# Kernel optimization log

Measured on AMD Instinct MI355X. Metric: run time of the kernel, lower is better.

Reference implementation:

```python
import jax, jax.numpy as jnp
import numpy as np

MODES = 4
WIDTH = 8
IN_CH = 3
OUT_CH = 6
LAMBDA_RES = 0.3


def spectral_conv3d(x, w1, w2, w3, w4):
    # x: [B, C, D, H, W] real. Standard FNO3d SpectralConv3d:
    # rfftn over last 3 dims, multiply low modes in 4 corner octants, irfftn.
    B, C, D, H, W = x.shape
    m = MODES
    x_ft = jnp.fft.rfftn(x, axes=(-3, -2, -1))  # [B,C,D,H,W//2+1] complex

    def mul(blk, w):
        return jnp.einsum('bixyz,ioxyz->boxyz', blk, w)

    out_ft = jnp.zeros((B, w1.shape[1], D, H, W // 2 + 1), dtype=x_ft.dtype)
    out_ft = out_ft.at[:, :, :m, :m, :m].set(mul(x_ft[:, :, :m, :m, :m], w1))
    out_ft = out_ft.at[:, :, -m:, :m, :m].set(mul(x_ft[:, :, -m:, :m, :m], w2))
    out_ft = out_ft.at[:, :, :m, -m:, :m].set(mul(x_ft[:, :, :m, -m:, :m], w3))
    out_ft = out_ft.at[:, :, -m:, -m:, :m].set(mul(x_ft[:, :, -m:, -m:, :m], w4))
    return jnp.fft.irfftn(out_ft, s=(D, H, W), axes=(-3, -2, -1))


def fno3d(u, fc0_w, fc0_b, spec_ws, conv_ws, conv_bs, fc1_w, fc1_b, fc2_w, fc2_b):
    # Lift: 1x1 conv via einsum (channels-first)
    x = jnp.einsum('bcdhw,oc->bodhw', u, fc0_w) + fc0_b[None, :, None, None, None]
    for i in range(4):
        w1, w2, w3, w4 = spec_ws[i]
        x1 = spectral_conv3d(x, w1, w2, w3, w4)
        x2 = jnp.einsum('bcdhw,oc->bodhw', x, conv_ws[i]) + conv_bs[i][None, :, None, None, None]
        x = x1 + x2
        if i < 3:
            x = jax.nn.gelu(x)
    x = jnp.einsum('bcdhw,oc->bodhw', x, fc1_w) + fc1_b[None, :, None, None, None]
    x = jax.nn.gelu(x)
    x = jnp.einsum('bcdhw,oc->bodhw', x, fc2_w) + fc2_b[None, :, None, None, None]
    return x


def setup_inputs() -> dict:
    key = jax.random.key(0)
    ks = jax.random.split(key, 32)
    B, D, H, W = 8, 64, 64, 64
    m, wd = MODES, WIDTH
    u = jax.random.normal(ks[0], (B, IN_CH, D, H, W), dtype=jnp.float32)
    scale = 1.0 / (wd * wd)
    spec_ws = []
    ki = 1
    for _ in range(4):
        layer = []
        for _ in range(4):
            re = jax.random.uniform(ks[ki], (wd, wd, m, m, m)) * scale
            im = jax.random.uniform(ks[ki + 1], (wd, wd, m, m, m)) * scale
            layer.append(re + 1j * im)
            ki += 2
        spec_ws.append(tuple(layer))
    conv_ws = [jax.random.normal(ks[ki + i], (wd, wd)) * (1.0 / wd) for i in range(4)]
    ki += 4
    conv_bs = [jnp.zeros((wd,), jnp.float32) for _ in range(4)]
    fc0_w = jax.random.normal(ks[ki], (wd, IN_CH)) * 0.3; ki += 1
    fc0_b = jnp.zeros((wd,), jnp.float32)
    fc1_w = jax.random.normal(ks[ki], (4 * wd, wd)) * 0.2; ki += 1
    fc1_b = jnp.zeros((4 * wd,), jnp.float32)
    fc2_w = jax.random.normal(ks[ki], (OUT_CH, 4 * wd)) * 0.2; ki += 1
    fc2_b = jnp.zeros((OUT_CH,), jnp.float32)
    nu = jnp.asarray(0.001, jnp.float32)
    return {
        'u': u, 'nu': nu,
        'fc0_w': fc0_w, 'fc0_b': fc0_b,
        'spec_ws': spec_ws, 'conv_ws': conv_ws, 'conv_bs': conv_bs,
        'fc1_w': fc1_w, 'fc1_b': fc1_b, 'fc2_w': fc2_w, 'fc2_b': fc2_b,
    }


def reference(u, nu, fc0_w, fc0_b, spec_ws, conv_ws, conv_bs, fc1_w, fc1_b, fc2_w, fc2_b):
    B, C, D, H, W = u.shape
    # hard core: zeros [B,6,D,H,W] with first 3 channels = u*nu
    hard = jnp.concatenate([u * nu, jnp.zeros((B, 3, D, H, W), u.dtype)], axis=1)
    soft = fno3d(u, fc0_w, fc0_b, spec_ws, conv_ws, conv_bs, fc1_w, fc1_b, fc2_w, fc2_b)
    return hard + LAMBDA_RES * soft
```

## Files before the change

kernel.cpp:

```cpp
#include <hip/hip_runtime.h>


#define TWO_PI_OVER_64 0.09817477042468103

__device__ __forceinline__ float gelu_fast(float x) {
    float x2 = x * x;
    float p  = x * (1.0f + 0.044715f * x2);
    float e  = __builtin_amdgcn_exp2f(-2.3022083f * p);
    return x * __builtin_amdgcn_rcpf(1.0f + e);
}

#define BUILD_TW() \
    __shared__ float twc[64], tws[64]; \
    if (threadIdx.x < 64) { \
        double a_ = TWO_PI_OVER_64 * (double)threadIdx.x; \
        twc[threadIdx.x] = (float)cos(a_); tws[threadIdx.x] = (float)sin(a_); \
    }

__device__ __forceinline__ void a_tail_lds(
    const float v[4], const float c1[4], const float s1[4],
    const float c2[4], const float s2[4], const float c3[4], const float s3[4],
    int wq, float4* __restrict__ AslRow)
{
    float p0  = v[0] + v[1] + v[2] + v[3];
    float ar1 = v[0]*c1[0] + v[1]*c1[1] + v[2]*c1[2] + v[3]*c1[3];
    float ai1 = -(v[0]*s1[0] + v[1]*s1[1] + v[2]*s1[2] + v[3]*s1[3]);
    float ar2 = v[0]*c2[0] + v[1]*c2[1] + v[2]*c2[2] + v[3]*c2[3];
    float ai2 = -(v[0]*s2[0] + v[1]*s2[1] + v[2]*s2[2] + v[3]*s2[3]);
    float ar3 = v[0]*c3[0] + v[1]*c3[1] + v[2]*c3[2] + v[3]*c3[3];
    float ai3 = -(v[0]*s3[0] + v[1]*s3[1] + v[2]*s3[2] + v[3]*s3[3]);
    #pragma unroll
    for (int m = 1; m < 16; m <<= 1) {
        p0  += __shfl_xor(p0,  m);
        ar1 += __shfl_xor(ar1, m);  ai1 += __shfl_xor(ai1, m);
        ar2 += __shfl_xor(ar2, m);  ai2 += __shfl_xor(ai2, m);
        ar3 += __shfl_xor(ar3, m);  ai3 += __shfl_xor(ai3, m);
    }
    if (wq < 2) {
        float4 av;
        av.x = (wq == 0) ? p0   : ar2;
        av.y = (wq == 0) ? 0.f  : ai2;
        av.z = (wq == 0) ? ar1  : ar3;
        av.w = (wq == 0) ? ai1  : ai3;
        AslRow[wq] = av;
    }
}

__device__ __forceinline__ void h_partial_atomic(
    const float2* __restrict__ Asl, const float* __restrict__ twc,
    const float* __restrict__ tws, int t, int b, int dx, int dy0,
    float2* __restrict__ Bh)
{
    const int kz = t & 3, ky = (t >> 2) & 7, o = t >> 5;
    const int kyv = ky < 4 ? ky : ky + 56;
    float re = 0.f, im = 0.f;
    int ti = (kyv * dy0) & 63;
    #pragma unroll
    for (int dyl = 0; dyl < 16; ++dyl) {
        float2 a = Asl[(o * 16 + dyl) * 4 + kz];
        float cc = twc[ti], ss = tws[ti];
        re += a.x * cc + a.y * ss;
        im += a.y * cc - a.x * ss;
        ti = (ti + kyv) & 63;
    }
    float* p = (float*)&Bh[(size_t)(b * 8 + o) * 2048 + dx * 32 + ky * 4 + kz];
    atomicAdd(p, re);
    atomicAdd(p + 1, im);
}

__global__ __launch_bounds__(256) void k_liftA(
    const float* __restrict__ u, const float* __restrict__ fc0w,
    const float* __restrict__ fc0b, float* __restrict__ x,
    float2* __restrict__ Bh)
{
    BUILD_TW();
    __shared__ float4 Asl4[8 * 16 * 2];
    const int t = threadIdx.x, bid = blockIdx.x;
    const int b = bid >> 8, dx = (bid >> 2) & 63, dy0 = (bid & 3) * 16;
    const int dyl = t >> 4, wq = t & 15;
    const size_t sp = (size_t)dx * 4096 + (size_t)(dy0 + dyl) * 64 + wq * 4;
    float uin[3][4];
    #pragma unroll
    for (int c = 0; c < 3; ++c) {
        float4 v = *(const float4*)&u[(size_t)(b * 3 + c) * 262144 + sp];
        uin[c][0] = v.x; uin[c][1] = v.y; uin[c][2] = v.z; uin[c][3] = v.w;
    }
    __syncthreads();
    float c1[4], s1[4], c2[4], s2[4], c3[4], s3[4];
    #pragma unroll
    for (int j = 0; j < 4; ++j) {
        int w = wq * 4 + j;
        c1[j] = twc[w];             s1[j] = tws[w];
        c2[j] = twc[(2 * w) & 63];  s2[j] = tws[(2 * w) & 63];
        c3[j] = twc[(3 * w) & 63];  s3[j] = tws[(3 * w) & 63];
    }
    #pragma unroll
    for (int o = 0; o < 8; ++o) {
        float w0 = fc0w[o * 3 + 0], w1 = fc0w[o * 3 + 1], w2 = fc0w[o * 3 + 2];
        float bb = fc0b[o];
        float v[4];
        #pragma unroll
        for (int j = 0; j < 4; ++j)
            v[j] = bb + uin[0][j] * w0 + uin[1][j] * w1 + uin[2][j] * w2;
        *(float4*)&x[(size_t)(b * 8 + o) * 262144 + sp] =
            make_float4(v[0], v[1], v[2], v[3]);
        a_tail_lds(v, c1, s1, c2, s2, c3, s3, wq, &Asl4[(o * 16 + dyl) * 2]);
    }
    __syncthreads();
    h_partial_atomic((const float2*)Asl4, twc, tws, t, b, dx, dy0, Bh);
}

__global__ __launch_bounds__(256) void k_fDmix(
    const float2* __restrict__ Bh,
    const float2* __restrict__ w1, const float2* __restrict__ w2,
    const float2* __restrict__ w3, const float2* __restrict__ w4,
    float2* __restrict__ O)
{
    BUILD_TW();
    __shared__ float2 Cs[256];
    const int t = threadIdx.x, bid = blockIdx.x;
    const int b = bid >> 3, kx = bid & 7;
    const int kxv = kx < 4 ? kx : kx + 56;
    __syncthreads();
    {
        int kz = t & 3, ky = (t >> 2) & 7, c = t >> 5;
        const float2* Bp = Bh + (size_t)(b * 8 + c) * 2048 + ky * 4 + kz;
        float re = 0.f, im = 0.f;
        int ti = 0;
        #pragma unroll 8
        for (int dx = 0; dx < 64; ++dx) {
            float2 v = Bp[dx * 32];
            float cc = twc[ti], ss = tws[ti];
            re += v.x * cc + v.y * ss;
            im += v.y * cc - v.x * ss;
            ti = (ti + kxv) & 63;
        }
        Cs[t] = make_float2(re, im);
    }
    __syncthreads();
    {
        int kz = t & 3, ky = (t >> 2) & 7, o = t >> 5;
        const float2* wsel = (kx < 4) ? ((ky < 4) ? w1 : w3) : ((ky < 4) ? w2 : w4);
        int kxw = kx & 3, kyw = ky & 3;
        float re = 0.f, im = 0.f;
        #pragma unroll
        for (int i = 0; i < 8; ++i) {
            float2 cv = Cs[i * 32 + ky * 4 + kz];
            float2 wv = wsel[(((size_t)(i * 8 + o) * 4 + kxw) * 4 + kyw) * 4 + kz];
            re += cv.x * wv.x - cv.y * wv.y;
            im += cv.x * wv.y + cv.y * wv.x;
        }
        O[(((size_t)(b * 8 + o) * 8 + kx) * 8 + ky) * 4 + kz] = make_float2(re, im);
    }
}

__global__ __launch_bounds__(256) void k_ptA(
    float* __restrict__ x, const float2* __restrict__ O,
    const float* __restrict__ cw, const float* __restrict__ cb,
    float2* __restrict__ Bh)
{
    BUILD_TW();
    __shared__ float2 Ps[256];
    __shared__ float2 Qs[8 * 16 * 4];
    __shared__ float4 Asl4[8 * 16 * 2];
    const int t = threadIdx.x, bid = blockIdx.x;
    const int b = bid >> 8, dx = (bid >> 2) & 63, dy0 = (bid & 3) * 16;
    const int dyl = t >> 4, wq = t & 15;
    const size_t sp = (size_t)dx * 4096 + (size_t)(dy0 + dyl) * 64 + wq * 4;
    float4 xv[8];
    #pragma unroll
    for (int c = 0; c < 8; ++c)
        xv[c] = *(const float4*)&x[(size_t)(b * 8 + c) * 262144 + sp];
    const int pkz = t & 3, pky = (t >> 2) & 7, po = t >> 5;
    float2 ov[8];
    #pragma unroll
    for (int kxi = 0; kxi < 8; ++kxi)
        ov[kxi] = O[(((size_t)(b * 8 + po) * 8 + kxi) * 8 + pky) * 4 + pkz];
    __syncthreads();
    {
        float re = 0.f, im = 0.f;
        #pragma unroll
        for (int kxi = 0; kxi < 8; ++kxi) {
            int kxv = kxi < 4 ? kxi : kxi + 56;
            int ti = (kxv * dx) & 63;
            float cc = twc[ti], ss = tws[ti];
            re += ov[kxi].x * cc - ov[kxi].y * ss;
            im += ov[kxi].y * cc + ov[kxi].x * ss;
        }
        Ps[t] = make_float2(re, im);
    }
    __syncthreads();
    for (int it = t; it < 512; it += 256) {
        int kz = it & 3, qdyl = (it >> 2) & 15, o = it >> 6;
        int dy = dy0 + qdyl;
        float re = 0.f, im = 0.f;
        #pragma unroll
        for (int kyi = 0; kyi < 8; ++kyi) {
            int kyv = kyi < 4 ? kyi : kyi + 56;
            int ti = (kyv * dy) & 63;
            float2 v = Ps[(o * 8 + kyi) * 4 + kz];
            float cc = twc[ti], ss = tws[ti];
            re += v.x * cc - v.y * ss;
            im += v.y * cc + v.x * ss;
        }
        Qs[(o * 16 + qdyl) * 4 + kz] = make_float2(re, im);
    }
    __syncthreads();
    float c1[4], s1[4], c2[4], s2[4], c3[4], s3[4];
    #pragma unroll
    for (int j = 0; j < 4; ++j) {
        int w = wq * 4 + j;
        c1[j] = twc[w];             s1[j] = tws[w];
        c2[j] = twc[(2 * w) & 63];  s2[j] = tws[(2 * w) & 63];
        c3[j] = twc[(3 * w) & 63];  s3[j] = tws[(3 * w) & 63];
    }
    const float invN3 = 1.0f / 262144.0f;
    #pragma unroll
    for (int o = 0; o < 8; ++o) {
        float4 qa = *(const float4*)&Qs[(o * 16 + dyl) * 4];
        float4 qb = *(const float4*)&Qs[(o * 16 + dyl) * 4 + 2];
        float outj[4];
        #pragma unroll
        for (int j = 0; j < 4; ++j) {
            float x1 = qa.x + 2.f * (qa.z * c1[j] - qa.w * s1[j]
                                   + qb.x * c2[j] - qb.y * s2[j]
                                   + qb.z * c3[j] - qb.w * s3[j]);
            x1 *= invN3;
            float x2 = cb[o];
            #pragma unroll
            for (int c = 0; c < 8; ++c) {
                const float* xc = &xv[c].x;
                x2 += cw[o * 8 + c] * xc[j];
            }
            outj[j] = gelu_fast(x1 + x2);
        }
        *(float4*)&x[(size_t)(b * 8 + o) * 262144 + sp] =
            make_float4(outj[0], outj[1], outj[2], outj[3]);
        a_tail_lds(outj, c1, s1, c2, s2, c3, s3, wq, &Asl4[(o * 16 + dyl) * 2]);
    }
    __syncthreads();
    h_partial_atomic((const float2*)Asl4, twc, tws, t, b, dx, dy0, Bh);
}

__global__ __launch_bounds__(256) void k_ptout(
    const float* __restrict__ x, const float2* __restrict__ O,
    const float* __restrict__ cw, const float* __restrict__ cb,
    const float* __restrict__ u, const float* __restrict__ nu,
    const float* __restrict__ fc1w, const float* __restrict__ fc1b,
    const float* __restrict__ fc2w, const float* __restrict__ fc2b,
    float* __restrict__ out)
{
    BUILD_TW();
    __shared__ float2 Ps[256];
    __shared__ float2 Qs[8 * 8 * 4];
    const int t = threadIdx.x, bid = blockIdx.x;
    const int b = bid >> 9, dx = (bid >> 3) & 63, dy0 = (bid & 7) * 8;
    const int dyl = t >> 5, wp = t & 31;
    const size_t sp = (size_t)dx * 4096 + (size_t)(dy0 + dyl) * 64 + wp * 2;
    float2 xv[8];
    #pragma unroll
    for (int c = 0; c < 8; ++c)
        xv[c] = *(const float2*)&x[(size_t)(b * 8 + c) * 262144 + sp];
    float2 uv[3];
    #pragma unroll
    for (int c = 0; c < 3; ++c)
        uv[c] = *(const float2*)&u[(size_t)(b * 3 + c) * 262144 + sp];
    const int pkz = t & 3, pky = (t >> 2) & 7, po = t >> 5;
    float2 ovv[8];
    #pragma unroll
    for (int kxi = 0; kxi < 8; ++kxi)
        ovv[kxi] = O[(((size_t)(b * 8 + po) * 8 + kxi) * 8 + pky) * 4 + pkz];
    __syncthreads();
    {
        float re = 0.f, im = 0.f;
        #pragma unroll
        for (int kxi = 0; kxi < 8; ++kxi) {
            int kxv = kxi < 4 ? kxi : kxi + 56;
            int ti = (kxv * dx) & 63;
            float cc = twc[ti], ss = tws[ti];
            re += ovv[kxi].x * cc - ovv[kxi].y * ss;
            im += ovv[kxi].y * cc + ovv[kxi].x * ss;
        }
        Ps[t] = make_float2(re, im);
    }
    __syncthreads();
    {
        int kz = t & 3, qdyl = (t >> 2) & 7, o = t >> 5;
        int dy = dy0 + qdyl;
        float re = 0.f, im = 0.f;
        #pragma unroll
        for (int kyi = 0; kyi < 8; ++kyi) {
            int kyv = kyi < 4 ? kyi : kyi + 56;
            int ti = (kyv * dy) & 63;
            float2 v = Ps[(o * 8 + kyi) * 4 + kz];
            float cc = twc[ti], ss = tws[ti];
            re += v.x * cc - v.y * ss;
            im += v.y * cc + v.x * ss;
        }
        Qs[(o * 8 + qdyl) * 4 + kz] = make_float2(re, im);
    }
    __syncthreads();
    float c1[2], s1[2], c2[2], s2[2], c3[2], s3[2];
    #pragma unroll
    for (int j = 0; j < 2; ++j) {
        int w = wp * 2 + j;
        c1[j] = twc[w];             s1[j] = tws[w];
        c2[j] = twc[(2 * w) & 63];  s2[j] = tws[(2 * w) & 63];
        c3[j] = twc[(3 * w) & 63];  s3[j] = tws[(3 * w) & 63];
    }
    const float invN3 = 1.0f / 262144.0f;
    float vv[8][2];
    #pragma unroll
    for (int o = 0; o < 8; ++o) {
        float4 qa = *(const float4*)&Qs[(o * 8 + dyl) * 4];
        float4 qb = *(const float4*)&Qs[(o * 8 + dyl) * 4 + 2];
        #pragma unroll
        for (int j = 0; j < 2; ++j) {
            float x1 = qa.x + 2.f * (qa.z * c1[j] - qa.w * s1[j]
                                   + qb.x * c2[j] - qb.y * s2[j]
                                   + qb.z * c3[j] - qb.w * s3[j]);
            x1 *= invN3;
            float x2 = cb[o];
            #pragma unroll
            for (int c = 0; c < 8; ++c) {
                const float* xc = &xv[c].x;
                x2 += cw[o * 8 + c] * xc[j];
            }
            vv[o][j] = x1 + x2;
        }
    }
    float so[6][2];
    #pragma unroll
    for (int c6 = 0; c6 < 6; ++c6)
        #pragma unroll
        for (int j = 0; j < 2; ++j) so[c6][j] = fc2b[c6];
    #pragma unroll 4
    for (int h = 0; h < 32; ++h) {
        float wr[8];
        #pragma unroll
        for (int c = 0; c < 8; ++c) wr[c] = fc1w[h * 8 + c];
        const float hb = fc1b[h];
        float w2r[6];
        #pragma unroll
        for (int c6 = 0; c6 < 6; ++c6) w2r[c6] = fc2w[c6 * 32 + h];
        #pragma unroll
        for (int j = 0; j < 2; ++j) {
            float a = hb;
            #pragma unroll
            for (int c = 0; c < 8; ++c) a += vv[c][j] * wr[c];
            float g = gelu_fast(a);
            #pragma unroll
            for (int c6 = 0; c6 < 6; ++c6) so[c6][j] += g * w2r[c6];
        }
    }
    const float nuv = nu[0];
    #pragma unroll
    for (int c6 = 0; c6 < 6; ++c6) {
        float2 res;
        if (c6 < 3) {
            res.x = 0.3f * so[c6][0] + uv[c6].x * nuv;
            res.y = 0.3f * so[c6][1] + uv[c6].y * nuv;
        } else {
            res.x = 0.3f * so[c6][0];
            res.y = 0.3f * so[c6][1];
        }
        *(float2*)&out[(size_t)(b * 6 + c6) * 262144 + sp] = res;
    }
}

__global__ void k_pack(const float* __restrict__ re, const float* __restrict__ im,
                       float2* __restrict__ dst)
{
    int i = blockIdx.x * 256 + threadIdx.x;
    if (i < 4096) dst[i] = make_float2(re[i], im[i]);
}

extern "C" void kernel_launch(void* const* d_in, const int* in_sizes, int n_in,
                              void* d_out, int out_size, void* d_ws, size_t ws_size,
                              hipStream_t stream)
{
    (void)out_size;
    const char* leaf[32];
    bool spec_split = false;
    const char* spec_re[16]; const char* spec_im[16];
    int src = 0;
    leaf[0] = (const char*)d_in[src++];
    leaf[1] = (const char*)d_in[src++];
    leaf[2] = (const char*)d_in[src++];
    leaf[3] = (const char*)d_in[src++];
    {
        int s = (src < n_in) ? in_sizes[src] : 4096;
        if (n_in >= 48 && s == 4096) {
            spec_split = true;
            for (int i = 0; i < 16; ++i) {
                spec_re[i] = (const char*)d_in[src++];
                spec_im[i] = (const char*)d_in[src++];
            }
        } else {
            int per;
            if (s == 4096 || s == 8192) per = 1;
            else if (s == 16384 || s == 32768) per = 4;
            else per = 16;
            for (int i = 0; i < 16; i += per) {
                const char* base = (const char*)d_in[src++];
                for (int j = 0; j < per; ++j) leaf[4 + i + j] = base + (size_t)j * 4096 * 8;
            }
        }
    }
    {
        int s = (src < n_in) ? in_sizes[src] : 64;
        if (s == 64) { for (int i = 0; i < 4; ++i) leaf[20 + i] = (const char*)d_in[src++]; }
        else { const char* base = (const char*)d_in[src++];
               for (int i = 0; i < 4; ++i) leaf[20 + i] = base + (size_t)i * 64 * 4; }
    }
    {
        int s = (src < n_in) ? in_sizes[src] : 8;
        if (s == 8) { for (int i = 0; i < 4; ++i) leaf[24 + i] = (const char*)d_in[src++]; }
        else { const char* base = (const char*)d_in[src++];
               for (int i = 0; i < 4; ++i) leaf[24 + i] = base + (size_t)i * 8 * 4; }
    }
    leaf[28] = (const char*)d_in[src++];
    leaf[29] = (const char*)d_in[src++];
    leaf[30] = (const char*)d_in[src++];
    leaf[31] = (const char*)d_in[src++];

    const float* u    = (const float*)leaf[0];
    const float* nu   = (const float*)leaf[1];
    const float* fc0w = (const float*)leaf[2];
    const float* fc0b = (const float*)leaf[3];
    const float* convw[4], *convb[4];
    for (int i = 0; i < 4; ++i) { convw[i] = (const float*)leaf[20 + i];
                                  convb[i] = (const float*)leaf[24 + i]; }
    const float* fc1w = (const float*)leaf[28];
    const float* fc1b = (const float*)leaf[29];
    const float* fc2w = (const float*)leaf[30];
    const float* fc2b = (const float*)leaf[31];

    const size_t szX = 67108864, szB = 1048576, szO = 131072, szSP = 524288;
    char* ws = (char*)d_ws;
    float* xbuf = (float*)ws;
    float2 *Bbuf, *Obuf, *SP;
    if (ws_size >= szX + szB + szO + szSP) {
        Bbuf = (float2*)(ws + szX);
        Obuf = (float2*)(ws + szX + szB);
        SP   = (float2*)(ws + szX + szB + szO);
    } else {
        Obuf = (float2*)(ws + szX);
        Bbuf = (float2*)d_out;
        SP   = (float2*)((char*)d_out + szB);
    }

    const float2* specw[16];
    if (spec_split) {
        for (int i = 0; i < 16; ++i) {
            hipLaunchKernelGGL(k_pack, dim3(16), dim3(256), 0, stream,
                               (const float*)spec_re[i], (const float*)spec_im[i],
                               SP + (size_t)i * 4096);
            specw[i] = SP + (size_t)i * 4096;
        }
    } else {
        for (int i = 0; i < 16; ++i) specw[i] = (const float2*)leaf[4 + i];
    }
    float* outp = (float*)d_out;

    hipMemsetAsync(Bbuf, 0, szB, stream);
    hipLaunchKernelGGL(k_liftA, dim3(2048), dim3(256), 0, stream, u, fc0w, fc0b, xbuf, Bbuf);
    for (int L = 0; L < 4; ++L) {
        hipLaunchKernelGGL(k_fDmix, dim3(64), dim3(256), 0, stream,
                           Bbuf, specw[L*4+0], specw[L*4+1], specw[L*4+2], specw[L*4+3], Obuf);
        if (L < 3) {
            hipMemsetAsync(Bbuf, 0, szB, stream);
            hipLaunchKernelGGL(k_ptA, dim3(2048), dim3(256), 0, stream,
                               xbuf, Obuf, convw[L], convb[L], Bbuf);
        } else {
            hipLaunchKernelGGL(k_ptout, dim3(4096), dim3(256), 0, stream,
                               xbuf, Obuf, convw[3], convb[3], u, nu,
                               fc1w, fc1b, fc2w, fc2b, outp);
        }
    }
}
```

Baseline: 315.2 us.

## Replace atomic partial-sum accumulation with per-slab stores and re-tile output kernel

The partial H-transform results are now written to four separate slabs (one per dy quarter) with plain stores instead of atomicAdd into one buffer. k_fDmix sums the four slabs while doing the D transform, which removes the atomics and the memset that preceded each layer. In exchange the workspace buffer grows fourfold and fDmix reads four times as much. Separately, k_ptout is re-tiled to one point per thread with twice the blocks, lowering per-thread register pressure.

```diff
diff --git a/kernel.cpp b/kernel.cpp
--- a/kernel.cpp
+++ b/kernel.cpp
@@ -46,10 +46,10 @@
     }
 }
 
-__device__ __forceinline__ void h_partial_atomic(
+__device__ __forceinline__ void h_partial_store(
     const float2* __restrict__ Asl, const float* __restrict__ twc,
     const float* __restrict__ tws, int t, int b, int dx, int dy0,
-    float2* __restrict__ Bh)
+    float2* __restrict__ BhSlab)
 {
     const int kz = t & 3, ky = (t >> 2) & 7, o = t >> 5;
     const int kyv = ky < 4 ? ky : ky + 56;
@@ -63,20 +63,18 @@
         im += a.y * cc - a.x * ss;
         ti = (ti + kyv) & 63;
     }
-    float* p = (float*)&Bh[(size_t)(b * 8 + o) * 2048 + dx * 32 + ky * 4 + kz];
-    atomicAdd(p, re);
-    atomicAdd(p + 1, im);
+    BhSlab[(size_t)(b * 8 + o) * 2048 + dx * 32 + ky * 4 + kz] = make_float2(re, im);
 }
 
 __global__ __launch_bounds__(256) void k_liftA(
     const float* __restrict__ u, const float* __restrict__ fc0w,
     const float* __restrict__ fc0b, float* __restrict__ x,
-    float2* __restrict__ Bh)
+    float2* __restrict__ BhP)
 {
     BUILD_TW();
     __shared__ float4 Asl4[8 * 16 * 2];
     const int t = threadIdx.x, bid = blockIdx.x;
-    const int b = bid >> 8, dx = (bid >> 2) & 63, dy0 = (bid & 3) * 16;
+    const int b = bid >> 8, dx = (bid >> 2) & 63, p = bid & 3, dy0 = p * 16;
     const int dyl = t >> 4, wq = t & 15;
     const size_t sp = (size_t)dx * 4096 + (size_t)(dy0 + dyl) * 64 + wq * 4;
     float uin[3][4];
@@ -107,11 +105,12 @@
         a_tail_lds(v, c1, s1, c2, s2, c3, s3, wq, &Asl4[(o * 16 + dyl) * 2]);
     }
     __syncthreads();
-    h_partial_atomic((const float2*)Asl4, twc, tws, t, b, dx, dy0, Bh);
+    h_partial_store((const float2*)Asl4, twc, tws, t, b, dx, dy0,
+                    BhP + (size_t)p * 131072);
 }
 
 __global__ __launch_bounds__(256) void k_fDmix(
-    const float2* __restrict__ Bh,
+    const float2* __restrict__ BhP,
     const float2* __restrict__ w1, const float2* __restrict__ w2,
     const float2* __restrict__ w3, const float2* __restrict__ w4,
     float2* __restrict__ O)
@@ -124,15 +123,18 @@
     __syncthreads();
     {
         int kz = t & 3, ky = (t >> 2) & 7, c = t >> 5;
-        const float2* Bp = Bh + (size_t)(b * 8 + c) * 2048 + ky * 4 + kz;
+        const float2* Bp = BhP + (size_t)(b * 8 + c) * 2048 + ky * 4 + kz;
         float re = 0.f, im = 0.f;
         int ti = 0;
-        #pragma unroll 8
+        #pragma unroll 4
         for (int dx = 0; dx < 64; ++dx) {
-            float2 v = Bp[dx * 32];
             float cc = twc[ti], ss = tws[ti];
-            re += v.x * cc + v.y * ss;
-            im += v.y * cc - v.x * ss;
+            #pragma unroll
+            for (int p = 0; p < 4; ++p) {
+                float2 v = Bp[(size_t)p * 131072 + dx * 32];
+                re += v.x * cc + v.y * ss;
+                im += v.y * cc - v.x * ss;
+            }
             ti = (ti + kxv) & 63;
         }
         Cs[t] = make_float2(re, im);
@@ -157,14 +159,14 @@
 __global__ __launch_bounds__(256) void k_ptA(
     float* __restrict__ x, const float2* __restrict__ O,
     const float* __restrict__ cw, const float* __restrict__ cb,
-    float2* __restrict__ Bh)
+    float2* __restrict__ BhP)
 {
     BUILD_TW();
     __shared__ float2 Ps[256];
     __shared__ float2 Qs[8 * 16 * 4];
     __shared__ float4 Asl4[8 * 16 * 2];
     const int t = threadIdx.x, bid = blockIdx.x;
-    const int b = bid >> 8, dx = (bid >> 2) & 63, dy0 = (bid & 3) * 16;
+    const int b = bid >> 8, dx = (bid >> 2) & 63, p = bid & 3, dy0 = p * 16;
     const int dyl = t >> 4, wq = t & 15;
     const size_t sp = (size_t)dx * 4096 + (size_t)(dy0 + dyl) * 64 + wq * 4;
     float4 xv[8];
@@ -239,7 +241,8 @@
         a_tail_lds(outj, c1, s1, c2, s2, c3, s3, wq, &Asl4[(o * 16 + dyl) * 2]);
     }
     __syncthreads();
-    h_partial_atomic((const float2*)Asl4, twc, tws, t, b, dx, dy0, Bh);
+    h_partial_store((const float2*)Asl4, twc, tws, t, b, dx, dy0,
+                    BhP + (size_t)p * 131072);
 }
 
 __global__ __launch_bounds__(256) void k_ptout(
@@ -252,19 +255,19 @@
 {
     BUILD_TW();
     __shared__ float2 Ps[256];
-    __shared__ float2 Qs[8 * 8 * 4];
+    __shared__ float2 Qs[8 * 4 * 4];
     const int t = threadIdx.x, bid = blockIdx.x;
-    const int b = bid >> 9, dx = (bid >> 3) & 63, dy0 = (bid & 7) * 8;
-    const int dyl = t >> 5, wp = t & 31;
-    const size_t sp = (size_t)dx * 4096 + (size_t)(dy0 + dyl) * 64 + wp * 2;
-    float2 xv[8];
+    const int b = bid >> 10, dx = (bid >> 4) & 63, dy0 = (bid & 15) * 4;
+    const int dyl = t >> 6, w = t & 63;
+    const size_t sp = (size_t)dx * 4096 + (size_t)(dy0 + dyl) * 64 + w;
+    float xv[8];
     #pragma unroll
     for (int c = 0; c < 8; ++c)
-        xv[c] = *(const float2*)&x[(size_t)(b * 8 + c) * 262144 + sp];
-    float2 uv[3];
+        xv[c] = x[(size_t)(b * 8 + c) * 262144 + sp];
+    float uvv[3];
     #pragma unroll
     for (int c = 0; c < 3; ++c)
-        uv[c] = *(const float2*)&u[(size_t)(b * 3 + c) * 262144 + sp];
+        uvv[c] = u[(size_t)(b * 3 + c) * 262144 + sp];
     const int pkz = t & 3, pky = (t >> 2) & 7, po = t >> 5;
     float2 ovv[8];
     #pragma unroll
@@ -284,8 +287,8 @@
         Ps[t] = make_float2(re, im);
     }
     __syncthreads();
-    {
-        int kz = t & 3, qdyl = (t >> 2) & 7, o = t >> 5;
+    if (t < 128) {
+        int kz = t & 3, qdyl = (t >> 2) & 3, o = t >> 4;
         int dy = dy0 + qdyl;
         float re = 0.f, im = 0.f;
         #pragma unroll
@@ -297,74 +300,45 @@
             re += v.x * cc - v.y * ss;
             im += v.y * cc + v.x * ss;
         }
-        Qs[(o * 8 + qdyl) * 4 + kz] = make_float2(re, im);
-    }
-    __syncthreads();
-    float c1[2], s1[2], c2[2], s2[2], c3[2], s3[2];
-    #pragma unroll
-    for (int j = 0; j < 2; ++j) {
-        int w = wp * 2 + j;
-        c1[j] = twc[w];             s1[j] = tws[w];
-        c2[j] = twc[(2 * w) & 63];  s2[j] = tws[(2 * w) & 63];
-        c3[j] = twc[(3 * w) & 63];  s3[j] = tws[(3 * w) & 63];
-    }
+        Qs[(o * 4 + qdyl) * 4 + kz] = make_float2(re, im);
+    }
+    __syncthreads();
+    const float tc1 = twc[w],           ts1 = tws[w];
+    const float tc2 = twc[(2 * w) & 63], ts2 = tws[(2 * w) & 63];
+    const float tc3 = twc[(3 * w) & 63], ts3 = tws[(3 * w) & 63];
     const float invN3 = 1.0f / 262144.0f;
-    float vv[8][2];
+    float vv[8];
     #pragma unroll
     for (int o = 0; o < 8; ++o) {
-        float4 qa = *(const float4*)&Qs[(o * 8 + dyl) * 4];
-        float4 qb = *(const float4*)&Qs[(o * 8 + dyl) * 4 + 2];
-        #pragma unroll
-        for (int j = 0; j < 2; ++j) {
-            float x1 = qa.x + 2.f * (qa.z * c1[j] - qa.w * s1[j]
-                                   + qb.x * c2[j] - qb.y * s2[j]
-                                   + qb.z * c3[j] - qb.w * s3[j]);
-            x1 *= invN3;
-            float x2 = cb[o];
-            #pragma unroll
-            for (int c = 0; c < 8; ++c) {
-                const float* xc = &xv[c].x;
-                x2 += cw[o * 8 + c] * xc[j];
-            }
-            vv[o][j] = x1 + x2;
-        }
-    }
-    float so[6][2];
-    #pragma unroll
-    for (int c6 = 0; c6 < 6; ++c6)
-        #pragma unroll
-        for (int j = 0; j < 2; ++j) so[c6][j] = fc2b[c6];
+        float4 qa = *(const float4*)&Qs[(o * 4 + dyl) * 4];
+        float4 qb = *(const float4*)&Qs[(o * 4 + dyl) * 4 + 2];
+        float x1 = qa.x + 2.f * (qa.z * tc1 - qa.w * ts1
+                               + qb.x * tc2 - qb.y * ts2
+                               + qb.z * tc3 - qb.w * ts3);
+        x1 *= invN3;
+        float x2 = cb[o];
+        #pragma unroll
+        for (int c = 0; c < 8; ++c) x2 += cw[o * 8 + c] * xv[c];
+        vv[o] = x1 + x2;
+    }
+    float so[6];
+    #pragma unroll
+    for (int c6 = 0; c6 < 6; ++c6) so[c6] = fc2b[c6];
     #pragma unroll 4
     for (int h = 0; h < 32; ++h) {
-        float wr[8];
-        #pragma unroll
-        for (int c = 0; c < 8; ++c) wr[c] = fc1w[h * 8 + c];
-        const float hb = fc1b[h];
-        float w2r[6];
-        #pragma unroll
-        for (int c6 = 0; c6 < 6; ++c6) w2r[c6] = fc2w[c6 * 32 + h];
-        #pragma unroll
-        for (int j = 0; j < 2; ++j) {
-            float a = hb;
-            #pragma unroll
-            for (int c = 0; c < 8; ++c) a += vv[c][j] * wr[c];
-            float g = gelu_fast(a);
-            #pragma unroll
-            for (int c6 = 0; c6 < 6; ++c6) so[c6][j] += g * w2r[c6];
-        }
+        float a = fc1b[h];
+        #pragma unroll
+        for (int c = 0; c < 8; ++c) a += vv[c] * fc1w[h * 8 + c];
+        float g = gelu_fast(a);
+        #pragma unroll
+        for (int c6 = 0; c6 < 6; ++c6) so[c6] += g * fc2w[c6 * 32 + h];
     }
     const float nuv = nu[0];
     #pragma unroll
     for (int c6 = 0; c6 < 6; ++c6) {
-        float2 res;
-        if (c6 < 3) {
-            res.x = 0.3f * so[c6][0] + uv[c6].x * nuv;
-            res.y = 0.3f * so[c6][1] + uv[c6].y * nuv;
-        } else {
-            res.x = 0.3f * so[c6][0];
-            res.y = 0.3f * so[c6][1];
-        }
-        *(float2*)&out[(size_t)(b * 6 + c6) * 262144 + sp] = res;
+        float res = 0.3f * so[c6];
+        if (c6 < 3) res += uvv[c6] * nuv;
+        out[(size_t)(b * 6 + c6) * 262144 + sp] = res;
     }
 }
 
@@ -436,7 +410,7 @@
     const float* fc2w = (const float*)leaf[30];
     const float* fc2b = (const float*)leaf[31];
 
-    const size_t szX = 67108864, szB = 1048576, szO = 131072, szSP = 524288;
+    const size_t szX = 67108864, szB = 4194304, szO = 131072, szSP = 524288;
     char* ws = (char*)d_ws;
     float* xbuf = (float*)ws;
     float2 *Bbuf, *Obuf, *SP;
@@ -463,17 +437,15 @@
     }
     float* outp = (float*)d_out;
 
-    hipMemsetAsync(Bbuf, 0, szB, stream);
     hipLaunchKernelGGL(k_liftA, dim3(2048), dim3(256), 0, stream, u, fc0w, fc0b, xbuf, Bbuf);
     for (int L = 0; L < 4; ++L) {
         hipLaunchKernelGGL(k_fDmix, dim3(64), dim3(256), 0, stream,
                            Bbuf, specw[L*4+0], specw[L*4+1], specw[L*4+2], specw[L*4+3], Obuf);
         if (L < 3) {
-            hipMemsetAsync(Bbuf, 0, szB, stream);
             hipLaunchKernelGGL(k_ptA, dim3(2048), dim3(256), 0, stream,
                                xbuf, Obuf, convw[L], convb[L], Bbuf);
         } else {
-            hipLaunchKernelGGL(k_ptout, dim3(4096), dim3(256), 0, stream,
+            hipLaunchKernelGGL(k_ptout, dim3(8192), dim3(256), 0, stream,
                                xbuf, Obuf, convw[3], convb[3], u, nu,
                                fc1w, fc1b, fc2w, fc2b, outp);
         }
```

Result: slower. 331.5 us (+5.2%).
